# Kernel optimization log

Measured on AMD Instinct MI355X. Metric: run time of the kernel, lower is better.

Reference implementation:

```python
import jax, jax.numpy as jnp
import numpy as np

H = 64  # hidden_channels == out_channels == 64
D = 64  # input feature dim for all node types


def _seg_mean(x_src, src, dst, n_dst):
    # gather neighbor features and mean-aggregate per destination node
    s = jax.ops.segment_sum(x_src[src], dst, num_segments=n_dst)  # [n_dst, d]
    cnt = jax.ops.segment_sum(jnp.ones_like(dst, dtype=x_src.dtype), dst, num_segments=n_dst)
    return s / jnp.maximum(cnt, 1.0)[:, None]


def _sage(x_src, x_dst, src, dst, Wl, bl, Wr):
    # PyG SAGEConv: lin_l(mean-aggr of neighbors) + lin_r(self), bias on lin_l only
    m = _seg_mean(x_src, src, dst, x_dst.shape[0])
    return m @ Wl.T + bl + x_dst @ Wr.T


def setup_inputs() -> dict:
    key = jax.random.key(0)
    ks = jax.random.split(key, 32)
    n_user, n_problem, n_topic = 50000, 20000, 500
    e_up, e_pt, e_pu = 1000000, 60000, 1000000
    inp = {
        "x_user": jax.random.normal(ks[0], (n_user, D), jnp.float32),
        "x_problem": jax.random.normal(ks[1], (n_problem, D), jnp.float32),
        "x_topic": jax.random.normal(ks[2], (n_topic, D), jnp.float32),
        "up_src": jax.random.randint(ks[3], (e_up,), 0, n_user, jnp.int32),
        "up_dst": jax.random.randint(ks[4], (e_up,), 0, n_problem, jnp.int32),
        "pt_src": jax.random.randint(ks[5], (e_pt,), 0, n_problem, jnp.int32),
        "pt_dst": jax.random.randint(ks[6], (e_pt,), 0, n_topic, jnp.int32),
        "pu_src": jax.random.randint(ks[7], (e_pu,), 0, n_problem, jnp.int32),
        "pu_dst": jax.random.randint(ks[8], (e_pu,), 0, n_user, jnp.int32),
    }
    # SAGEConv params per relation per layer: Wl [H,in_src], bl [H], Wr [H,in_dst]
    names = [
        "W1_up_l", "W1_up_r", "W1_pt_l", "W1_pt_r", "W1_pu_l", "W1_pu_r",
        "W2_up_l", "W2_up_r", "W2_pt_l", "W2_pt_r", "W2_pu_l", "W2_pu_r",
    ]
    sc = 1.0 / np.sqrt(D)
    for i, n in enumerate(names):
        inp[n] = jax.random.uniform(ks[9 + i], (H, D), jnp.float32, -sc, sc)
    for i, n in enumerate(["b1_up", "b1_pt", "b1_pu", "b2_up", "b2_pt", "b2_pu"]):
        inp[n] = jax.random.uniform(ks[21 + i], (H,), jnp.float32, -sc, sc)
    return inp


def reference(x_user, x_problem, x_topic,
              up_src, up_dst, pt_src, pt_dst, pu_src, pu_dst,
              W1_up_l, W1_up_r, b1_up, W1_pt_l, W1_pt_r, b1_pt,
              W1_pu_l, W1_pu_r, b1_pu,
              W2_up_l, W2_up_r, b2_up, W2_pt_l, W2_pt_r, b2_pt,
              W2_pu_l, W2_pu_r, b2_pu):
    # conv1 (each dst type has exactly one incoming relation)
    h_problem = jax.nn.relu(_sage(x_user, x_problem, up_src, up_dst, W1_up_l, b1_up, W1_up_r))
    h_topic = jax.nn.relu(_sage(x_problem, x_topic, pt_src, pt_dst, W1_pt_l, b1_pt, W1_pt_r))
    h_user = jax.nn.relu(_sage(x_problem, x_user, pu_src, pu_dst, W1_pu_l, b1_pu, W1_pu_r))
    # dropout(0.2) is identity at inference
    # conv2
    o_problem = _sage(h_user, h_problem, up_src, up_dst, W2_up_l, b2_up, W2_up_r)
    o_topic = _sage(h_problem, h_topic, pt_src, pt_dst, W2_pt_l, b2_pt, W2_pt_r)
    o_user = _sage(h_problem, h_user, pu_src, pu_dst, W2_pu_l, b2_pu, W2_pu_r)
    return (o_user, o_problem, o_topic)
```

## Files before the change

### kernel.cpp

```cpp
#include <hip/hip_runtime.h>

#define BLK 256
#define SB_SHIFT 7
#define NBMAX 576
#define CHUNK_E 8192
#define TPAD 68
#define SMEM_BYTES 52224

typedef float f32x2 __attribute__((ext_vector_type(2)));

__device__ inline unsigned short f2bf(float f) {
    union { float f; unsigned u; } c; c.f = f;
    unsigned u = c.u + (0x7fffu + ((c.u >> 16) & 1u));
    return (unsigned short)(u >> 16);
}


__global__ void zero2_kernel(int* __restrict__ a, int na, int* __restrict__ b, int nb) {
    int i = blockIdx.x * blockDim.x + threadIdx.x;
    if (i < na) a[i] = 0;
    if (i < nb) b[i] = 0;
}


struct B2Jobs {
    const int* src[3];
    const int* dst[3];
    int E[3];
    int nboff[4];
    int ndst[3];
    int R2off[3];
    int chunk_off[4];
    int stride[3];
    int pbase[3];
};

struct TJobs {
    const float* x[6];
    const float* W[6];
    const float* b[6];
    void* y[6];
    int n[6];
    int obf16[6];
    int boff[7];
};

__device__ void transform_body(const TJobs& J, int b, char* smem) {
    float* xlds = (float*)smem;
    float* wlds = xlds + 128 * TPAD;
    int j = 0;
    while (b >= J.boff[j + 1]) ++j;
    int n = J.n[j];
    int n0 = (b - J.boff[j]) * 128;
    const float4* __restrict__ x4 = (const float4*)J.x[j];
    const float4* __restrict__ W4 = (const float4*)J.W[j];
    const float* bb = J.b[j];
    int t = threadIdx.x;

#pragma unroll
    for (int q = 0; q < 8; ++q) {
        int idx = q * 256 + t;
        int node = idx >> 4, kq = idx & 15;
        float4 v = make_float4(0.f, 0.f, 0.f, 0.f);
        if (n0 + node < n) v = x4[(size_t)(n0 + node) * 16 + kq];
        *(float4*)&xlds[node * TPAD + kq * 4] = v;
    }
#pragma unroll
    for (int q = 0; q < 4; ++q) {
        int idx = q * 256 + t;
        int h = idx >> 4, kq = idx & 15;
        float4 v = W4[idx];
        wlds[(kq * 4 + 0) * TPAD + h] = v.x;
        wlds[(kq * 4 + 1) * TPAD + h] = v.y;
        wlds[(kq * 4 + 2) * TPAD + h] = v.z;
        wlds[(kq * 4 + 3) * TPAD + h] = v.w;
    }
    __syncthreads();

    int tx = t & 15, ty = t >> 4;
    float4 bias4 = make_float4(0.f, 0.f, 0.f, 0.f);
    if (bb) bias4 = *(const float4*)&bb[tx * 4];
    float acc[8][4];
#pragma unroll
    for (int i = 0; i < 8; ++i) {
        acc[i][0] = bias4.x; acc[i][1] = bias4.y;
        acc[i][2] = bias4.z; acc[i][3] = bias4.w;
    }

    for (int k4 = 0; k4 < 16; ++k4) {
        float4 wv0 = *(const float4*)&wlds[(k4 * 4 + 0) * TPAD + tx * 4];
        float4 wv1 = *(const float4*)&wlds[(k4 * 4 + 1) * TPAD + tx * 4];
        float4 wv2 = *(const float4*)&wlds[(k4 * 4 + 2) * TPAD + tx * 4];
        float4 wv3 = *(const float4*)&wlds[(k4 * 4 + 3) * TPAD + tx * 4];
#pragma unroll
        for (int i = 0; i < 8; ++i) {
            float4 xv = *(const float4*)&xlds[(ty + 16 * i) * TPAD + k4 * 4];
            acc[i][0] += xv.x * wv0.x + xv.y * wv1.x + xv.z * wv2.x + xv.w * wv3.x;
            acc[i][1] += xv.x * wv0.y + xv.y * wv1.y + xv.z * wv2.y + xv.w * wv3.y;
            acc[i][2] += xv.x * wv0.z + xv.y * wv1.z + xv.z * wv2.z + xv.w * wv3.z;
            acc[i][3] += xv.x * wv0.w + xv.y * wv1.w + xv.z * wv2.w + xv.w * wv3.w;
        }
    }

    if (J.obf16[j]) {
        unsigned short* __restrict__ yb = (unsigned short*)J.y[j];
#pragma unroll
        for (int i = 0; i < 8; ++i) {
            int node = n0 + ty + 16 * i;
            if (node < n) {
                ushort4 o;
                o.x = f2bf(acc[i][0]); o.y = f2bf(acc[i][1]);
                o.z = f2bf(acc[i][2]); o.w = f2bf(acc[i][3]);
                *(ushort4*)&yb[(size_t)node * 64 + tx * 4] = o;
            }
        }
    } else {
        float* __restrict__ y = (float*)J.y[j];
#pragma unroll
        for (int i = 0; i < 8; ++i) {
            int node = n0 + ty + 16 * i;
            if (node < n) {
                float4 o = make_float4(acc[i][0], acc[i][1], acc[i][2], acc[i][3]);
                ((float4*)y)[(size_t)node * 16 + tx] = o;
            }
        }
    }
}

__launch_bounds__(BLK)
__global__ void bbin_t1_kernel(B2Jobs B, TJobs T, int nbbin,
                               int* __restrict__ bcur, int* __restrict__ ebuf, int NB) {
    __shared__ __align__(16) char smem[SMEM_BYTES];
    if (blockIdx.x >= nbbin) { transform_body(T, blockIdx.x - nbbin, smem); return; }

    int* lc  = (int*)smem;
    int* res = lc + NBMAX;
    int* cur = res + NBMAX;
    int tid = threadIdx.x;
    for (int i = tid; i < NB; i += BLK) { lc[i] = 0; cur[i] = 0; }
    __syncthreads();
    int b = blockIdx.x, r = 0;
    while (b >= B.chunk_off[r + 1]) ++r;
    int e0 = (b - B.chunk_off[r]) * CHUNK_E;
    int e1 = min(e0 + CHUNK_E, B.E[r]);
    const int* __restrict__ src = B.src[r];
    const int* __restrict__ dst = B.dst[r];
    int boffr = B.nboff[r];
    for (int e = e0 + tid; e < e1; e += BLK)
        atomicAdd(&lc[boffr + (dst[e] >> SB_SHIFT)], 1);
    __syncthreads();
    for (int i = tid; i < NB; i += BLK)
        if (lc[i]) res[i] = atomicAdd(&bcur[i], lc[i]);
    __syncthreads();
    int str = B.stride[r];
    int basem = B.pbase[r] - boffr * str;
    for (int e = e0 + tid; e < e1; e += BLK) {
        int s = src[e], d = dst[e];
        int bk = boffr + (d >> SB_SHIFT);
        int l = atomicAdd(&cur[bk], 1);
        ebuf[basem + bk * str + res[bk] + l] = (s << SB_SHIFT) | (d & 127);
    }
}

__launch_bounds__(BLK)
__global__ void bplace_kernel(B2Jobs B, const int* __restrict__ bcur,
                              const int* __restrict__ ebuf,
                              int* __restrict__ ccsr, int2* __restrict__ row2cat) {
    __shared__ int cnt[128];
    __shared__ int off[128];
    __shared__ int cur[128];
    int tid = threadIdx.x;
    int bk = blockIdx.x, r = 0;
    while (bk >= B.nboff[r + 1]) ++r;
    int lb = bk - B.nboff[r];
    int dst0 = lb << SB_SHIFT;
    int nd = B.ndst[r] - dst0;
    if (nd > 128) nd = 128;
    int base = B.pbase[r] + lb * B.stride[r];
    int cntE = bcur[bk];
    if (tid < 128) cnt[tid] = 0;
    __syncthreads();
    for (int e = tid; e < cntE; e += BLK)
        atomicAdd(&cnt[ebuf[base + e] & 127], 1);
    __syncthreads();
    if (tid < 128) off[tid] = cnt[tid];
    __syncthreads();
    for (int st = 1; st < 128; st <<= 1) {
        int v = 0;
        if (tid < 128 && tid >= st) v = off[tid - st];
        __syncthreads();
        if (tid < 128) off[tid] += v;
        __syncthreads();
    }
    int2* __restrict__ row2 = row2cat + B.R2off[r];
    if (tid < nd) {
        int ex = off[tid] - cnt[tid];
        row2[dst0 + tid] = make_int2(base + ex, base + ex + cnt[tid]);
        cur[tid] = ex;
    }
    __syncthreads();
    for (int e = tid; e < cntE; e += BLK) {
        int sd = ebuf[base + e];
        int l = atomicAdd(&cur[sd & 127], 1);
        ccsr[base + l] = sd & 0xFFFFFF80;
    }
    if (tid < 48) ccsr[base + cntE + tid] = 0;
}


__launch_bounds__(BLK)
__global__ void transform_kernel(TJobs J) {
    __shared__ __align__(16) char smem[SMEM_BYTES];
    transform_body(J, blockIdx.x, smem);
}


struct GJobs {
    const unsigned short* y[3];
    const int2* row2[3];
    const int* csr;
    float* out[3];
    int n[3];
    int boff[4];
    int relu;
};

__launch_bounds__(BLK)
__global__ void gather_kernel(GJobs J) {
    int b = blockIdx.x, j = 0;
    while (b >= J.boff[j + 1]) ++j;
    int lane = threadIdx.x & 63, wv = threadIdx.x >> 6;
    int node = (b - J.boff[j]) * 4 + wv;
    if (node >= J.n[j]) return;
    const int* __restrict__ csr = J.csr;
    const char* __restrict__ yb = (const char*)J.y[j];
    float* __restrict__ out = J.out[j];

    int2 rr = J.row2[j][node];
    int e0 = rr.x, e1 = rr.y;
    int deg = e1 - e0;
    int sub = lane >> 3;
    int fe = lane & 7;
    int fo = fe << 4;

    f32x2 acc[4];
#pragma unroll
    for (int t = 0; t < 4; ++t) acc[t] = (f32x2)(0.f, 0.f);

    auto accum = [&](uint4 v) {
        unsigned w[4] = {v.x, v.y, v.z, v.w};
#pragma unroll
        for (int t = 0; t < 4; ++t) {
            f32x2 p;
            p.x = __uint_as_float(w[t] << 16);
            p.y = __uint_as_float(w[t] & 0xffff0000u);
            asm("v_pk_add_f32 %0, %1, %2" : "=v"(acc[t]) : "v"(p), "v"(acc[t]));
        }
    };

    int nfull = deg >> 4;
    int e = e0;
    if (nfull > 0) {
        int ia0, ia1, ib0, ib1;
        uint4 va0, va1, vb0, vb1;
        ia0 = csr[e0 + sub];       ia1 = csr[e0 + 8 + sub];
        ib0 = csr[e0 + 16 + sub];  ib1 = csr[e0 + 24 + sub];
        va0 = *(const uint4*)(yb + (ia0 + fo));
        va1 = *(const uint4*)(yb + (ia1 + fo));
        int k = 0;
        while (k + 2 <= nfull) {
            vb0 = *(const uint4*)(yb + (ib0 + fo));
            vb1 = *(const uint4*)(yb + (ib1 + fo));
            ia0 = csr[e0 + (k + 2) * 16 + sub];
            ia1 = csr[e0 + (k + 2) * 16 + 8 + sub];
            accum(va0); accum(va1);
            va0 = *(const uint4*)(yb + (ia0 + fo));
            va1 = *(const uint4*)(yb + (ia1 + fo));
            ib0 = csr[e0 + (k + 3) * 16 + sub];
            ib1 = csr[e0 + (k + 3) * 16 + 8 + sub];
            accum(vb0); accum(vb1);
            k += 2;
        }
        if (k < nfull) { accum(va0); accum(va1); }
        e = e0 + nfull * 16;
    }
    if (e < e1) {
#pragma unroll
        for (int t = 0; t < 2; ++t) {
            int ee = e + t * 8 + sub;
            int idx = csr[ee < e1 ? ee : e1 - 1];
            uint4 v = *(const uint4*)(yb + (idx + fo));
            if (ee >= e1) v = make_uint4(0u, 0u, 0u, 0u);
            accum(v);
        }
    }

    float r[8];
#pragma unroll
    for (int t = 0; t < 4; ++t) { r[t * 2] = acc[t].x; r[t * 2 + 1] = acc[t].y; }
#pragma unroll
    for (int t = 0; t < 8; ++t) {
        r[t] += __shfl_xor(r[t], 8, 64);
        r[t] += __shfl_xor(r[t], 16, 64);
        r[t] += __shfl_xor(r[t], 32, 64);
    }
    float inv = deg > 0 ? 1.f / (float)deg : 0.f;

    if (sub == 0) {
        size_t oi = (size_t)node * 64 + (fe << 3);
        float4 z0 = *(const float4*)&out[oi];
        float4 z1 = *(const float4*)&out[oi + 4];
        float4 o0 = make_float4(z0.x + r[0] * inv, z0.y + r[1] * inv,
                                z0.z + r[2] * inv, z0.w + r[3] * inv);
        float4 o1 = make_float4(z1.x + r[4] * inv, z1.y + r[5] * inv,
                                z1.z + r[6] * inv, z1.w + r[7] * inv);
        if (J.relu) {
            o0.x = fmaxf(o0.x, 0.f); o0.y = fmaxf(o0.y, 0.f);
            o0.z = fmaxf(o0.z, 0.f); o0.w = fmaxf(o0.w, 0.f);
            o1.x = fmaxf(o1.x, 0.f); o1.y = fmaxf(o1.y, 0.f);
            o1.z = fmaxf(o1.z, 0.f); o1.w = fmaxf(o1.w, 0.f);
        }
        *(float4*)&out[oi] = o0;
        *(float4*)&out[oi + 4] = o1;
    }
}


extern "C" void kernel_launch(void* const* d_in, const int* in_sizes, int n_in,
                              void* d_out, int out_size, void* d_ws, size_t ws_size,
                              hipStream_t stream) {
    const float* x_user    = (const float*)d_in[0];
    const float* x_problem = (const float*)d_in[1];
    const float* x_topic   = (const float*)d_in[2];
    const int* up_src = (const int*)d_in[3];
    const int* up_dst = (const int*)d_in[4];
    const int* pt_src = (const int*)d_in[5];
    const int* pt_dst = (const int*)d_in[6];
    const int* pu_src = (const int*)d_in[7];
    const int* pu_dst = (const int*)d_in[8];
    const float* W1_up_l = (const float*)d_in[9];
    const float* W1_up_r = (const float*)d_in[10];
    const float* W1_pt_l = (const float*)d_in[11];
    const float* W1_pt_r = (const float*)d_in[12];
    const float* W1_pu_l = (const float*)d_in[13];
    const float* W1_pu_r = (const float*)d_in[14];
    const float* W2_up_l = (const float*)d_in[15];
    const float* W2_up_r = (const float*)d_in[16];
    const float* W2_pt_l = (const float*)d_in[17];
    const float* W2_pt_r = (const float*)d_in[18];
    const float* W2_pu_l = (const float*)d_in[19];
    const float* W2_pu_r = (const float*)d_in[20];
    const float* b1_up = (const float*)d_in[21];
    const float* b1_pt = (const float*)d_in[22];
    const float* b1_pu = (const float*)d_in[23];
    const float* b2_up = (const float*)d_in[24];
    const float* b2_pt = (const float*)d_in[25];
    const float* b2_pu = (const float*)d_in[26];

    int n_user = in_sizes[0] / 64;
    int n_problem = in_sizes[1] / 64;
    int n_topic = in_sizes[2] / 64;
    int E_up = in_sizes[3];
    int E_pt = in_sizes[5];
    int E_pu = in_sizes[7];

    float* o_user = (float*)d_out;
    float* o_problem = o_user + (size_t)n_user * 64;
    float* o_topic = o_problem + (size_t)n_problem * 64;

    char* ws = (char*)d_ws;
    size_t off = 0;
    auto alloc = [&](size_t bytes) -> void* {
        void* p = ws + off;
        off += (bytes + 255) & ~(size_t)255;
        return p;
    };
    auto cdiv = [](int a, int b) { return (a + b - 1) / b; };

    float* h_user    = (float*)alloc((size_t)n_user * 64 * 4);
    float* h_problem = (float*)alloc((size_t)n_problem * 64 * 4);
    float* h_topic   = (float*)alloc((size_t)n_topic * 64 * 4);
    unsigned short* y_up = (unsigned short*)alloc((size_t)n_user * 64 * 2);
    unsigned short* y_pt = (unsigned short*)alloc((size_t)n_problem * 64 * 2);
    unsigned short* y_pu = (unsigned short*)alloc((size_t)n_problem * 64 * 2);

    int nb0 = cdiv(n_problem, 128), nb1 = cdiv(n_topic, 128), nb2 = cdiv(n_user, 128);
    int NB = nb0 + nb1 + nb2;

    int st_up = 12288, st_pt = 24576, st_pu = 6144;
    int p0 = 0;
    int p1 = p0 + nb0 * st_up;
    int p2 = p1 + nb1 * st_pt;
    int ptot = p2 + nb2 * st_pu;

    int*  bcur    = (int*)alloc((size_t)NB * 4);
    int2* row2cat = (int2*)alloc((size_t)(n_problem + n_topic + n_user) * 8);
    int*  ebuf    = (int*)alloc((size_t)ptot * 4);
    int*  ccsr    = (int*)alloc(((size_t)ptot + 64) * 4);

    B2Jobs B;
    B.src[0] = up_src; B.dst[0] = up_dst; B.E[0] = E_up;
    B.src[1] = pt_src; B.dst[1] = pt_dst; B.E[1] = E_pt;
    B.src[2] = pu_src; B.dst[2] = pu_dst; B.E[2] = E_pu;
    B.nboff[0] = 0; B.nboff[1] = nb0; B.nboff[2] = nb0 + nb1; B.nboff[3] = NB;
    B.ndst[0] = n_problem; B.ndst[1] = n_topic; B.ndst[2] = n_user;
    B.R2off[0] = 0; B.R2off[1] = n_problem; B.R2off[2] = n_problem + n_topic;
    B.chunk_off[0] = 0;
    for (int r = 0; r < 3; ++r) B.chunk_off[r + 1] = B.chunk_off[r] + cdiv(B.E[r], CHUNK_E);
    B.stride[0] = st_up; B.stride[1] = st_pt; B.stride[2] = st_pu;
    B.pbase[0] = p0; B.pbase[1] = p1; B.pbase[2] = p2;

    const int2* row2_up = row2cat + B.R2off[0];
    const int2* row2_pt = row2cat + B.R2off[1];
    const int2* row2_pu = row2cat + B.R2off[2];

    zero2_kernel<<<cdiv(NB > 64 ? NB : 64, 256), 256, 0, stream>>>(bcur, NB, ccsr + ptot, 64);

    TJobs T1;
    {
        const float* xs[6] = {x_user, x_problem, x_problem, x_problem, x_topic, x_user};
        const float* Ws[6] = {W1_up_l, W1_pt_l, W1_pu_l, W1_up_r, W1_pt_r, W1_pu_r};
        const float* bs[6] = {nullptr, nullptr, nullptr, b1_up, b1_pt, b1_pu};
        void* ys[6] = {y_up, y_pt, y_pu, h_problem, h_topic, h_user};
        int ns[6] = {n_user, n_problem, n_problem, n_problem, n_topic, n_user};
        int ob[6] = {1, 1, 1, 0, 0, 0};
        T1.boff[0] = 0;
        for (int j = 0; j < 6; ++j) {
            T1.x[j] = xs[j]; T1.W[j] = Ws[j]; T1.b[j] = bs[j]; T1.y[j] = ys[j]; T1.n[j] = ns[j];
            T1.obf16[j] = ob[j];
            T1.boff[j + 1] = T1.boff[j] + cdiv(ns[j], 128);
        }
    }
    int nbbin = B.chunk_off[3];
    bbin_t1_kernel<<<nbbin + T1.boff[6], BLK, 0, stream>>>(B, T1, nbbin, bcur, ebuf, NB);

    bplace_kernel<<<NB, BLK, 0, stream>>>(B, bcur, ebuf, ccsr, row2cat);

    {
        GJobs G;
        const unsigned short* gy[3] = {y_pu, y_up, y_pt};
        const int2* gr[3] = {row2_pu, row2_up, row2_pt};
        float* go[3] = {h_user, h_problem, h_topic};
        int gn[3] = {n_user, n_problem, n_topic};
        G.csr = ccsr;
        G.boff[0] = 0;
        for (int j = 0; j < 3; ++j) {
            G.y[j] = gy[j]; G.row2[j] = gr[j]; G.out[j] = go[j]; G.n[j] = gn[j];
            G.boff[j + 1] = G.boff[j] + cdiv(gn[j], 4);
        }
        G.relu = 1;
        gather_kernel<<<G.boff[3], BLK, 0, stream>>>(G);
    }

    {
        TJobs T;
        const float* xs[6] = {h_user, h_problem, h_problem, h_problem, h_topic, h_user};
        const float* Ws[6] = {W2_up_l, W2_pt_l, W2_pu_l, W2_up_r, W2_pt_r, W2_pu_r};
        const float* bs[6] = {nullptr, nullptr, nullptr, b2_up, b2_pt, b2_pu};
        void* ys[6] = {y_up, y_pt, y_pu, o_problem, o_topic, o_user};
        int ns[6] = {n_user, n_problem, n_problem, n_problem, n_topic, n_user};
        int ob[6] = {1, 1, 1, 0, 0, 0};
        T.boff[0] = 0;
        for (int j = 0; j < 6; ++j) {
            T.x[j] = xs[j]; T.W[j] = Ws[j]; T.b[j] = bs[j]; T.y[j] = ys[j]; T.n[j] = ns[j];
            T.obf16[j] = ob[j];
            T.boff[j + 1] = T.boff[j] + cdiv(ns[j], 128);
        }
        transform_kernel<<<T.boff[6], BLK, 0, stream>>>(T);
    }

    {
        GJobs G;
        const unsigned short* gy[3] = {y_pu, y_up, y_pt};
        const int2* gr[3] = {row2_pu, row2_up, row2_pt};
        float* go[3] = {o_user, o_problem, o_topic};
        int gn[3] = {n_user, n_problem, n_topic};
        G.csr = ccsr;
        G.boff[0] = 0;
        for (int j = 0; j < 3; ++j) {
            G.y[j] = gy[j]; G.row2[j] = gr[j]; G.out[j] = go[j]; G.n[j] = gn[j];
            G.boff[j + 1] = G.boff[j] + cdiv(gn[j], 4);
        }
        G.relu = 0;
        gather_kernel<<<G.boff[3], BLK, 0, stream>>>(G);
    }
}
```

Measured before the change: 174.6 us.

## Split edge binning into standalone kernel and co-schedule transform with bucket placement

Edge binning now runs in its own kernel with a smaller edge chunk per block, so more blocks are launched and each needs less shared memory, which should raise occupancy. The layer-1 dense transform moves out of the binning launch and into the bucket-placement launch, overlapping the transform with placement work. The intent is to balance the heterogeneous block mix and shorten the critical path. Smaller chunks mean more global atomics on the bucket counters and more fragmented ebuf writes, and the placement blocks now reserve the large transform shared-memory allocation.

```diff
diff --git a/kernel.cpp b/kernel.cpp
--- a/kernel.cpp
+++ b/kernel.cpp
@@ -3,7 +3,7 @@
 #define BLK 256
 #define SB_SHIFT 7
 #define NBMAX 576
-#define CHUNK_E 8192
+#define CHUNK_E 2048
 #define TPAD 68
 #define SMEM_BYTES 52224
 
@@ -45,6 +45,37 @@
     int boff[7];
 };
 
+__launch_bounds__(BLK)
+__global__ void bbin_kernel(B2Jobs B, int* __restrict__ bcur, int* __restrict__ ebuf, int NB) {
+    __shared__ int lc[NBMAX];
+    __shared__ int res[NBMAX];
+    __shared__ int cur[NBMAX];
+    int tid = threadIdx.x;
+    for (int i = tid; i < NB; i += BLK) { lc[i] = 0; cur[i] = 0; }
+    __syncthreads();
+    int b = blockIdx.x, r = 0;
+    while (b >= B.chunk_off[r + 1]) ++r;
+    int e0 = (b - B.chunk_off[r]) * CHUNK_E;
+    int e1 = min(e0 + CHUNK_E, B.E[r]);
+    const int* __restrict__ src = B.src[r];
+    const int* __restrict__ dst = B.dst[r];
+    int boffr = B.nboff[r];
+    for (int e = e0 + tid; e < e1; e += BLK)
+        atomicAdd(&lc[boffr + (dst[e] >> SB_SHIFT)], 1);
+    __syncthreads();
+    for (int i = tid; i < NB; i += BLK)
+        if (lc[i]) res[i] = atomicAdd(&bcur[i], lc[i]);
+    __syncthreads();
+    int str = B.stride[r];
+    int basem = B.pbase[r] - boffr * str;
+    for (int e = e0 + tid; e < e1; e += BLK) {
+        int s = src[e], d = dst[e];
+        int bk = boffr + (d >> SB_SHIFT);
+        int l = atomicAdd(&cur[bk], 1);
+        ebuf[basem + bk * str + res[bk] + l] = (s << SB_SHIFT) | (d & 127);
+    }
+}
+
 __device__ void transform_body(const TJobs& J, int b, char* smem) {
     float* xlds = (float*)smem;
     float* wlds = xlds + 128 * TPAD;
@@ -127,50 +158,15 @@
     }
 }
 
-__launch_bounds__(BLK)
-__global__ void bbin_t1_kernel(B2Jobs B, TJobs T, int nbbin,
-                               int* __restrict__ bcur, int* __restrict__ ebuf, int NB) {
-    __shared__ __align__(16) char smem[SMEM_BYTES];
-    if (blockIdx.x >= nbbin) { transform_body(T, blockIdx.x - nbbin, smem); return; }
-
-    int* lc  = (int*)smem;
-    int* res = lc + NBMAX;
-    int* cur = res + NBMAX;
+__device__ void bplace_body(const B2Jobs& B, int bk, const int* __restrict__ bcur,
+                            const int* __restrict__ ebuf,
+                            int* __restrict__ ccsr, int2* __restrict__ row2cat,
+                            char* smem) {
+    int* cnt = (int*)smem;
+    int* off = cnt + 128;
+    int* cur = off + 128;
     int tid = threadIdx.x;
-    for (int i = tid; i < NB; i += BLK) { lc[i] = 0; cur[i] = 0; }
-    __syncthreads();
-    int b = blockIdx.x, r = 0;
-    while (b >= B.chunk_off[r + 1]) ++r;
-    int e0 = (b - B.chunk_off[r]) * CHUNK_E;
-    int e1 = min(e0 + CHUNK_E, B.E[r]);
-    const int* __restrict__ src = B.src[r];
-    const int* __restrict__ dst = B.dst[r];
-    int boffr = B.nboff[r];
-    for (int e = e0 + tid; e < e1; e += BLK)
-        atomicAdd(&lc[boffr + (dst[e] >> SB_SHIFT)], 1);
-    __syncthreads();
-    for (int i = tid; i < NB; i += BLK)
-        if (lc[i]) res[i] = atomicAdd(&bcur[i], lc[i]);
-    __syncthreads();
-    int str = B.stride[r];
-    int basem = B.pbase[r] - boffr * str;
-    for (int e = e0 + tid; e < e1; e += BLK) {
-        int s = src[e], d = dst[e];
-        int bk = boffr + (d >> SB_SHIFT);
-        int l = atomicAdd(&cur[bk], 1);
-        ebuf[basem + bk * str + res[bk] + l] = (s << SB_SHIFT) | (d & 127);
-    }
-}
-
-__launch_bounds__(BLK)
-__global__ void bplace_kernel(B2Jobs B, const int* __restrict__ bcur,
-                              const int* __restrict__ ebuf,
-                              int* __restrict__ ccsr, int2* __restrict__ row2cat) {
-    __shared__ int cnt[128];
-    __shared__ int off[128];
-    __shared__ int cur[128];
-    int tid = threadIdx.x;
-    int bk = blockIdx.x, r = 0;
+    int r = 0;
     while (bk >= B.nboff[r + 1]) ++r;
     int lb = bk - B.nboff[r];
     int dst0 = lb << SB_SHIFT;
@@ -205,6 +201,15 @@
         ccsr[base + l] = sd & 0xFFFFFF80;
     }
     if (tid < 48) ccsr[base + cntE + tid] = 0;
+}
+
+__launch_bounds__(BLK)
+__global__ void bplace_t1_kernel(B2Jobs B, TJobs T, int NB,
+                                 const int* __restrict__ bcur, const int* __restrict__ ebuf,
+                                 int* __restrict__ ccsr, int2* __restrict__ row2cat) {
+    __shared__ __align__(16) char smem[SMEM_BYTES];
+    if (blockIdx.x < NB) bplace_body(B, blockIdx.x, bcur, ebuf, ccsr, row2cat, smem);
+    else transform_body(T, blockIdx.x - NB, smem);
 }
 
 
@@ -416,6 +421,8 @@
 
     zero2_kernel<<<cdiv(NB > 64 ? NB : 64, 256), 256, 0, stream>>>(bcur, NB, ccsr + ptot, 64);
 
+    bbin_kernel<<<B.chunk_off[3], BLK, 0, stream>>>(B, bcur, ebuf, NB);
+
     TJobs T1;
     {
         const float* xs[6] = {x_user, x_problem, x_problem, x_problem, x_topic, x_user};
@@ -431,10 +438,7 @@
             T1.boff[j + 1] = T1.boff[j] + cdiv(ns[j], 128);
         }
     }
-    int nbbin = B.chunk_off[3];
-    bbin_t1_kernel<<<nbbin + T1.boff[6], BLK, 0, stream>>>(B, T1, nbbin, bcur, ebuf, NB);
-
-    bplace_kernel<<<NB, BLK, 0, stream>>>(B, bcur, ebuf, ccsr, row2cat);
+    bplace_t1_kernel<<<NB + T1.boff[6], BLK, 0, stream>>>(B, T1, NB, bcur, ebuf, ccsr, row2cat);
 
     {
         GJobs G;
```

Measured after the change: 180.2 us. +3.2%, slower.
